# Optimization experiments

Measured on AMD Instinct MI355X. Metric: run time of the kernel, lower is better.

## Reference

```python
import jax, jax.numpy as jnp
import numpy as np

D_MODEL = 512
MAX_LEN = 4096
B, P, Q = 32, 2048, 2048
VOCABS = (7, 24, 288)


def _make_pe(max_len, d):
    # pe[pos, 2k] = sin(pos / 10000**(2k/d)), pe[pos, 2k+1] = cos(same angle)
    pos = jnp.arange(max_len, dtype=jnp.float32)[:, None]
    i = jnp.arange(0, d, 2, dtype=jnp.float32)
    ang = pos / jnp.power(10000.0, i / d)          # [max_len, d/2]
    pe = jnp.stack([jnp.sin(ang), jnp.cos(ang)], axis=-1).reshape(max_len, d)
    return pe


def setup_inputs() -> dict:
    key = jax.random.key(0)
    ks = jax.random.split(key, 12)
    inp = {}
    names = ["in0", "tg0", "in1", "tg1", "in2", "tg2"]
    vocabs = [7, 7, 24, 24, 288, 288]
    for n, v, k in zip(names, vocabs, ks[:6]):
        inp[n] = jax.random.randint(k, (B, P), 0, v, dtype=jnp.int64 if jax.config.jax_enable_x64 else jnp.int32)
    inp["emb0"] = jax.random.normal(ks[6], (VOCABS[0], D_MODEL), jnp.float32) * 0.02
    inp["emb1"] = jax.random.normal(ks[7], (VOCABS[1], D_MODEL), jnp.float32) * 0.02
    inp["emb2"] = jax.random.normal(ks[8], (VOCABS[2], D_MODEL), jnp.float32) * 0.02
    inp["pe"] = _make_pe(MAX_LEN, D_MODEL)
    fan_in = (len(VOCABS) + 1) * D_MODEL
    bound = 1.0 / np.sqrt(fan_in)
    inp["W"] = jax.random.uniform(ks[9], (fan_in, D_MODEL), jnp.float32, -bound, bound)
    inp["b"] = jax.random.uniform(ks[10], (D_MODEL,), jnp.float32, -bound, bound)
    return inp


def reference(in0, tg0, in1, tg1, in2, tg2, emb0, emb1, emb2, pe, W, b):
    def encode(i0, i1, i2):
        Bk, L = i0.shape
        pos = jnp.broadcast_to(pe[:L], (Bk, L, pe.shape[1]))
        feats = jnp.concatenate([emb0[i0], emb1[i1], emb2[i2], pos], axis=-1)  # [B, L, 4*d]
        return feats @ W + b                                                   # [B, L, d]

    return encode(in0, in1, in2), encode(tg0, tg1, tg2)
```

## Files before the change

kernel.cpp:

```cpp
#include <hip/hip_runtime.h>


#define TILE 64
#define TKK  16

__global__ __launch_bounds__(256) void te_table_gemm(
    const float* __restrict__ emb0, const float* __restrict__ emb1,
    const float* __restrict__ emb2, const float* __restrict__ pe,
    const float* __restrict__ W, const float* __restrict__ bias,
    float* __restrict__ T)
{
    __shared__ float As[TKK][TILE + 4];
    __shared__ float Bs[TKK][TILE + 4];

    const int nt  = blockIdx.x;
    const int mt  = blockIdx.y;
    const int tid = threadIdx.x;

    const float* A; int M; int m0; int wrow; float* outp; bool addb;
    if (mt == 0)      { A = emb0; M = 7;    m0 = 0;              wrow = 0;    outp = T;           addb = false; }
    else if (mt == 1) { A = emb1; M = 24;   m0 = 0;              wrow = 512;  outp = T + 7*512;   addb = false; }
    else if (mt < 7)  { A = emb2; M = 288;  m0 = (mt - 2)*TILE;  wrow = 1024; outp = T + 31*512;  addb = false; }
    else              { A = pe;   M = 2048; m0 = (mt - 7)*TILE;  wrow = 1536; outp = T + 319*512; addb = true;  }

    const int n0 = nt * TILE;

    const int ar = tid >> 2;
    const int ac = (tid & 3) * 4;
    const int br = tid >> 4;
    const int bc = (tid & 15) * 4;

    const int my = (tid >> 4) * 4;
    const int mx = (tid & 15) * 4;

    float acc[4][4];
    #pragma unroll
    for (int i = 0; i < 4; i++)
        #pragma unroll
        for (int j = 0; j < 4; j++) acc[i][j] = 0.f;

    for (int k0 = 0; k0 < 512; k0 += TKK) {
        float4 av = make_float4(0.f, 0.f, 0.f, 0.f);
        if (m0 + ar < M)
            av = *(const float4*)&A[(size_t)(m0 + ar) * 512 + k0 + ac];
        float4 bv = *(const float4*)&W[(size_t)(wrow + k0 + br) * 512 + n0 + bc];

        __syncthreads();
        As[ac + 0][ar] = av.x;
        As[ac + 1][ar] = av.y;
        As[ac + 2][ar] = av.z;
        As[ac + 3][ar] = av.w;
        *(float4*)&Bs[br][bc] = bv;
        __syncthreads();

        #pragma unroll
        for (int k = 0; k < TKK; k++) {
            float4 a4 = *(const float4*)&As[k][my];
            float4 b4 = *(const float4*)&Bs[k][mx];
            acc[0][0] += a4.x * b4.x; acc[0][1] += a4.x * b4.y; acc[0][2] += a4.x * b4.z; acc[0][3] += a4.x * b4.w;
            acc[1][0] += a4.y * b4.x; acc[1][1] += a4.y * b4.y; acc[1][2] += a4.y * b4.z; acc[1][3] += a4.y * b4.w;
            acc[2][0] += a4.z * b4.x; acc[2][1] += a4.z * b4.y; acc[2][2] += a4.z * b4.z; acc[2][3] += a4.z * b4.w;
            acc[3][0] += a4.w * b4.x; acc[3][1] += a4.w * b4.y; acc[3][2] += a4.w * b4.z; acc[3][3] += a4.w * b4.w;
        }
    }

    float4 bb = make_float4(0.f, 0.f, 0.f, 0.f);
    if (addb) bb = *(const float4*)&bias[n0 + mx];

    #pragma unroll
    for (int i = 0; i < 4; i++) {
        int row = m0 + my + i;
        if (row < M) {
            float4 v;
            v.x = acc[i][0] + bb.x;
            v.y = acc[i][1] + bb.y;
            v.z = acc[i][2] + bb.z;
            v.w = acc[i][3] + bb.w;
            *(float4*)&outp[(size_t)row * 512 + n0 + mx] = v;
        }
    }
}

__global__ __launch_bounds__(256) void te_gather_add(
    const int* __restrict__ in0, const int* __restrict__ tg0,
    const int* __restrict__ in1, const int* __restrict__ tg1,
    const int* __restrict__ in2, const int* __restrict__ tg2,
    const float* __restrict__ T, float* __restrict__ out)
{
    const int gid = blockIdx.x * 256 + threadIdx.x;
    const int d4  = gid & 127;
    const int row = gid >> 7;
    const int l   = row & 2047;
    const int bl  = row & 65535;
    const int o   = row >> 16;

    const int* __restrict__ p0 = o ? tg0 : in0;
    const int* __restrict__ p1 = o ? tg1 : in1;
    const int* __restrict__ p2 = o ? tg2 : in2;
    const int i0 = p0[bl];
    const int i1 = p1[bl];
    const int i2 = p2[bl];

    const float4* __restrict__ T0 = (const float4*)T;
    const float4* __restrict__ T1 = (const float4*)(T + 7 * 512);
    const float4* __restrict__ T2 = (const float4*)(T + 31 * 512);
    const float4* __restrict__ Tp = (const float4*)(T + 319 * 512);

    const float4 a = T0[i0 * 128 + d4];
    const float4 b = T1[i1 * 128 + d4];
    const float4 c = T2[i2 * 128 + d4];
    const float4 p = Tp[l  * 128 + d4];

    float4 r;
    r.x = a.x + b.x + c.x + p.x;
    r.y = a.y + b.y + c.y + p.y;
    r.z = a.z + b.z + c.z + p.z;
    r.w = a.w + b.w + c.w + p.w;

    ((float4*)out)[gid] = r;
}

extern "C" void kernel_launch(void* const* d_in, const int* in_sizes, int n_in,
                              void* d_out, int out_size, void* d_ws, size_t ws_size,
                              hipStream_t stream) {
    const int*   in0  = (const int*)  d_in[0];
    const int*   tg0  = (const int*)  d_in[1];
    const int*   in1  = (const int*)  d_in[2];
    const int*   tg1  = (const int*)  d_in[3];
    const int*   in2  = (const int*)  d_in[4];
    const int*   tg2  = (const int*)  d_in[5];
    const float* emb0 = (const float*)d_in[6];
    const float* emb1 = (const float*)d_in[7];
    const float* emb2 = (const float*)d_in[8];
    const float* pe   = (const float*)d_in[9];
    const float* W    = (const float*)d_in[10];
    const float* bias = (const float*)d_in[11];
    float* out = (float*)d_out;
    float* T   = (float*)d_ws;

    dim3 ggrid(8, 39);
    te_table_gemm<<<ggrid, 256, 0, stream>>>(emb0, emb1, emb2, pe, W, bias, T);

    te_gather_add<<<65536, 256, 0, stream>>>(in0, tg0, in1, tg1, in2, tg2, T, out);
}
```

Baseline: 380.7 us.

## Split-K the table GEMM with smaller tiles, add reduce kernel, nontemporal output stores

The table GEMM now uses 32x64 tiles and splits K into four slices, launching 2400 blocks instead of 312 so the small GEMM fills the GPU. Each slice writes partial sums to workspace, and a new reduce kernel sums them and adds the bias. The gather-add kernel's large output write now uses nontemporal stores to avoid cache pollution. The cost is an extra kernel launch plus the write and read of partial-sum traffic.

Result: faster. 359.1 us (-5.7%).

```diff
diff --git a/kernel.cpp b/kernel.cpp
--- a/kernel.cpp
+++ b/kernel.cpp
@@ -1,84 +1,109 @@
 #include <hip/hip_runtime.h>
 
 
-#define TILE 64
-#define TKK  16
+#define TM 32
+#define TN 64
+#define TK 16
+#define KSPLIT 4
+#define TROWS 2367
 
-__global__ __launch_bounds__(256) void te_table_gemm(
+typedef float vfloat4 __attribute__((ext_vector_type(4)));
+
+__global__ __launch_bounds__(256) void te_gemm_partial(
     const float* __restrict__ emb0, const float* __restrict__ emb1,
     const float* __restrict__ emb2, const float* __restrict__ pe,
-    const float* __restrict__ W, const float* __restrict__ bias,
-    float* __restrict__ T)
+    const float* __restrict__ W, float* __restrict__ P)
 {
-    __shared__ float As[TKK][TILE + 4];
-    __shared__ float Bs[TKK][TILE + 4];
+    __shared__ float As[TK][TM + 4];
+    __shared__ float Bs[TK][TN + 4];
 
     const int nt  = blockIdx.x;
     const int mt  = blockIdx.y;
+    const int kz  = blockIdx.z;
     const int tid = threadIdx.x;
 
-    const float* A; int M; int m0; int wrow; float* outp; bool addb;
-    if (mt == 0)      { A = emb0; M = 7;    m0 = 0;              wrow = 0;    outp = T;           addb = false; }
-    else if (mt == 1) { A = emb1; M = 24;   m0 = 0;              wrow = 512;  outp = T + 7*512;   addb = false; }
-    else if (mt < 7)  { A = emb2; M = 288;  m0 = (mt - 2)*TILE;  wrow = 1024; outp = T + 31*512;  addb = false; }
-    else              { A = pe;   M = 2048; m0 = (mt - 7)*TILE;  wrow = 1536; outp = T + 319*512; addb = true;  }
+    const float* A; int M; int m0; int wrow; int tbase;
+    if (mt == 0)       { A = emb0; M = 7;    m0 = 0;            wrow = 0;    tbase = 0;   }
+    else if (mt == 1)  { A = emb1; M = 24;   m0 = 0;            wrow = 512;  tbase = 7;   }
+    else if (mt < 11)  { A = emb2; M = 288;  m0 = (mt-2)*TM;    wrow = 1024; tbase = 31;  }
+    else               { A = pe;   M = 2048; m0 = (mt-11)*TM;   wrow = 1536; tbase = 319; }
 
-    const int n0 = nt * TILE;
+    const int n0 = nt * TN;
+    const int kbase = kz * 128;
 
     const int ar = tid >> 2;
     const int ac = (tid & 3) * 4;
     const int br = tid >> 4;
     const int bc = (tid & 15) * 4;
 
-    const int my = (tid >> 4) * 4;
+    const int my = (tid >> 4) * 2;
     const int mx = (tid & 15) * 4;
 
-    float acc[4][4];
+    float acc[2][4];
     #pragma unroll
-    for (int i = 0; i < 4; i++)
+    for (int i = 0; i < 2; i++)
         #pragma unroll
         for (int j = 0; j < 4; j++) acc[i][j] = 0.f;
 
-    for (int k0 = 0; k0 < 512; k0 += TKK) {
+    for (int k0 = 0; k0 < 128; k0 += TK) {
         float4 av = make_float4(0.f, 0.f, 0.f, 0.f);
-        if (m0 + ar < M)
-            av = *(const float4*)&A[(size_t)(m0 + ar) * 512 + k0 + ac];
-        float4 bv = *(const float4*)&W[(size_t)(wrow + k0 + br) * 512 + n0 + bc];
+        if (ar < TM && (m0 + ar) < M)
+            av = *(const float4*)&A[(size_t)(m0 + ar) * 512 + kbase + k0 + ac];
+        float4 bv = *(const float4*)&W[(size_t)(wrow + kbase + k0 + br) * 512 + n0 + bc];
 
         __syncthreads();
-        As[ac + 0][ar] = av.x;
-        As[ac + 1][ar] = av.y;
-        As[ac + 2][ar] = av.z;
-        As[ac + 3][ar] = av.w;
+        if (ar < TM) {
+            As[ac + 0][ar] = av.x;
+            As[ac + 1][ar] = av.y;
+            As[ac + 2][ar] = av.z;
+            As[ac + 3][ar] = av.w;
+        }
         *(float4*)&Bs[br][bc] = bv;
         __syncthreads();
 
         #pragma unroll
-        for (int k = 0; k < TKK; k++) {
-            float4 a4 = *(const float4*)&As[k][my];
+        for (int k = 0; k < TK; k++) {
+            float2 a2 = *(const float2*)&As[k][my];
             float4 b4 = *(const float4*)&Bs[k][mx];
-            acc[0][0] += a4.x * b4.x; acc[0][1] += a4.x * b4.y; acc[0][2] += a4.x * b4.z; acc[0][3] += a4.x * b4.w;
-            acc[1][0] += a4.y * b4.x; acc[1][1] += a4.y * b4.y; acc[1][2] += a4.y * b4.z; acc[1][3] += a4.y * b4.w;
-            acc[2][0] += a4.z * b4.x; acc[2][1] += a4.z * b4.y; acc[2][2] += a4.z * b4.z; acc[2][3] += a4.z * b4.w;
-            acc[3][0] += a4.w * b4.x; acc[3][1] += a4.w * b4.y; acc[3][2] += a4.w * b4.z; acc[3][3] += a4.w * b4.w;
+            acc[0][0] += a2.x * b4.x; acc[0][1] += a2.x * b4.y;
+            acc[0][2] += a2.x * b4.z; acc[0][3] += a2.x * b4.w;
+            acc[1][0] += a2.y * b4.x; acc[1][1] += a2.y * b4.y;
+            acc[1][2] += a2.y * b4.z; acc[1][3] += a2.y * b4.w;
         }
     }
 
-    float4 bb = make_float4(0.f, 0.f, 0.f, 0.f);
-    if (addb) bb = *(const float4*)&bias[n0 + mx];
-
     #pragma unroll
-    for (int i = 0; i < 4; i++) {
+    for (int i = 0; i < 2; i++) {
         int row = m0 + my + i;
         if (row < M) {
-            float4 v;
-            v.x = acc[i][0] + bb.x;
-            v.y = acc[i][1] + bb.y;
-            v.z = acc[i][2] + bb.z;
-            v.w = acc[i][3] + bb.w;
-            *(float4*)&outp[(size_t)row * 512 + n0 + mx] = v;
+            *(float4*)&P[((size_t)kz * TROWS + tbase + row) * 512 + n0 + mx] =
+                make_float4(acc[i][0], acc[i][1], acc[i][2], acc[i][3]);
         }
     }
+}
+
+__global__ __launch_bounds__(256) void te_reduce(
+    const float* __restrict__ P, const float* __restrict__ bias,
+    float* __restrict__ T)
+{
+    const int idx4 = blockIdx.x * 256 + threadIdx.x;
+    if (idx4 >= TROWS * 128) return;
+    const int row = idx4 >> 7;
+    const int d4  = idx4 & 127;
+
+    const float4* P4 = (const float4*)P;
+    const size_t stride4 = (size_t)TROWS * 128;
+    float4 s = P4[idx4];
+    #pragma unroll
+    for (int kz = 1; kz < KSPLIT; kz++) {
+        float4 v = P4[kz * stride4 + idx4];
+        s.x += v.x; s.y += v.y; s.z += v.z; s.w += v.w;
+    }
+    if (row >= 319) {
+        float4 bb = ((const float4*)bias)[d4];
+        s.x += bb.x; s.y += bb.y; s.z += bb.z; s.w += bb.w;
+    }
+    ((float4*)T)[idx4] = s;
 }
 
 __global__ __launch_bounds__(256) void te_gather_add(
@@ -111,13 +136,13 @@
     const float4 c = T2[i2 * 128 + d4];
     const float4 p = Tp[l  * 128 + d4];
 
-    float4 r;
+    vfloat4 r;
     r.x = a.x + b.x + c.x + p.x;
     r.y = a.y + b.y + c.y + p.y;
     r.z = a.z + b.z + c.z + p.z;
     r.w = a.w + b.w + c.w + p.w;
 
-    ((float4*)out)[gid] = r;
+    __builtin_nontemporal_store(r, ((vfloat4*)out) + gid);
 }
 
 extern "C" void kernel_launch(void* const* d_in, const int* in_sizes, int n_in,
@@ -137,9 +162,12 @@
     const float* bias = (const float*)d_in[11];
     float* out = (float*)d_out;
     float* T   = (float*)d_ws;
+    float* P   = T + (size_t)TROWS * 512;
 
-    dim3 ggrid(8, 39);
-    te_table_gemm<<<ggrid, 256, 0, stream>>>(emb0, emb1, emb2, pe, W, bias, T);
+    dim3 ggrid(8, 75, KSPLIT);
+    te_gemm_partial<<<ggrid, 256, 0, stream>>>(emb0, emb1, emb2, pe, W, P);
+
+    te_reduce<<<(TROWS * 128 + 255) / 256, 256, 0, stream>>>(P, bias, T);
 
     te_gather_add<<<65536, 256, 0, stream>>>(in0, tg0, in1, tg1, in2, tg2, T, out);
 }
```
